# Optimization experiments

Hardware: AMD Instinct MI355X
Metric: run time of the kernel (lower is better)

## Reference

```python
import jax, jax.numpy as jnp
import numpy as np

N, E, G = 40000, 640000, 32
H, HEADS, L, O = 128, 4, 4, 100
C = H // HEADS


def setup_inputs() -> dict:
    key = jax.random.key(0)
    ks = iter(jax.random.split(key, 40))
    def w(shape, fan):
        return jax.random.normal(next(ks), shape, jnp.float32) / np.float32(np.sqrt(fan))
    inp = {}
    inp["x"] = jax.random.normal(next(ks), (N, 4), jnp.float32)
    inp["edge_attr"] = jax.random.normal(next(ks), (E, 5), jnp.float32)
    inp["node_w"] = w((4, H), 4); inp["node_b"] = jnp.zeros((H,), jnp.float32)
    inp["edge_w"] = w((5, H), 5); inp["edge_b"] = jnp.zeros((H,), jnp.float32)
    inp["Wq"] = w((L, H, H), H); inp["bq"] = jnp.zeros((L, H), jnp.float32)
    inp["Wk"] = w((L, H, H), H); inp["bk"] = jnp.zeros((L, H), jnp.float32)
    inp["Wv"] = w((L, H, H), H); inp["bv"] = jnp.zeros((L, H), jnp.float32)
    inp["We"] = w((L, H, H), H)  # lin_edge has bias=False in PyG TransformerConv
    inp["Wskip"] = w((L, H, H), H); inp["bskip"] = jnp.zeros((L, H), jnp.float32)
    inp["ln_g"] = jnp.ones((L, H), jnp.float32); inp["ln_b"] = jnp.zeros((L, H), jnp.float32)
    inp["dos_w1"] = w((H, H // 2), H); inp["dos_b1"] = jnp.zeros((H // 2,), jnp.float32)
    inp["dos_w2"] = w((H // 2, O), H // 2); inp["dos_b2"] = jnp.zeros((O,), jnp.float32)
    inp["tr_w1"] = w((H, H // 2), H); inp["tr_b1"] = jnp.zeros((H // 2,), jnp.float32)
    inp["tr_w2"] = w((H // 2, O), H // 2); inp["tr_b2"] = jnp.zeros((O,), jnp.float32)
    inp["edge_index"] = jax.random.randint(next(ks), (2, E), 0, N, jnp.int32)
    inp["batch"] = jnp.sort(jax.random.randint(next(ks), (N,), 0, G, jnp.int32))
    return inp


def _seg_softmax(a, seg, n):
    # numerically stable scatter-softmax over edges grouped by destination node
    m = jax.ops.segment_max(a, seg, num_segments=n)
    e = jnp.exp(a - m[seg])
    s = jax.ops.segment_sum(e, seg, num_segments=n)
    return e / (s[seg] + 1e-16)


def _layer_norm(x, g, b, eps=1e-5):
    mu = x.mean(-1, keepdims=True)
    var = ((x - mu) ** 2).mean(-1, keepdims=True)
    return (x - mu) * jax.lax.rsqrt(var + eps) * g + b


def _forward(x, edge_attr, node_w, node_b, edge_w, edge_b, Wq, bq, Wk, bk, Wv, bv,
             We, Wskip, bskip, ln_g, ln_b,
             dos_w1, dos_b1, dos_w2, dos_b2, tr_w1, tr_b1, tr_w2, tr_b2,
             edge_index, batch):
    src, dst = edge_index[0], edge_index[1]  # PyG default flow: source->target
    n = x.shape[0]
    h = x @ node_w + node_b        # [N, H] node_proj
    e_h = edge_attr @ edge_w + edge_b  # [E, H] edge_proj (shared across layers)
    scale = np.float32(1.0 / np.sqrt(C))
    for i in range(L):  # TransformerConv -> LayerNorm -> ReLU (dropout is eval-mode no-op)
        q = (h @ Wq[i] + bq[i]).reshape(n, HEADS, C)
        k = (h @ Wk[i] + bk[i]).reshape(n, HEADS, C)
        v = (h @ Wv[i] + bv[i]).reshape(n, HEADS, C)
        e = (e_h @ We[i]).reshape(-1, HEADS, C)
        kj = k[src] + e            # [E, heads, C]
        vj = v[src] + e
        alpha = jnp.sum(q[dst] * kj, axis=-1) * scale  # [E, heads]
        alpha = _seg_softmax(alpha, dst, n)
        msg = vj * alpha[..., None]
        out = jax.ops.segment_sum(msg, dst, num_segments=n).reshape(n, H)
        out = out + h @ Wskip[i] + bskip[i]  # root_weight skip
        h = jax.nn.relu(_layer_norm(out, ln_g[i], ln_b[i]))
    # global mean pool per graph
    sums = jax.ops.segment_sum(h, batch, num_segments=G)
    cnt = jax.ops.segment_sum(jnp.ones((n, 1), h.dtype), batch, num_segments=G)
    hg = sums / jnp.maximum(cnt, 1.0)
    dos = jax.nn.relu(hg @ dos_w1 + dos_b1) @ dos_w2 + dos_b2
    tr = jax.nn.relu(hg @ tr_w1 + tr_b1) @ tr_w2 + tr_b2
    return dos, tr


def reference(x, edge_attr, node_w, node_b, edge_w, edge_b, Wq, bq, Wk, bk, Wv, bv,
              We, Wskip, bskip, ln_g, ln_b,
              dos_w1, dos_b1, dos_w2, dos_b2, tr_w1, tr_b1, tr_w2, tr_b2,
              edge_index, batch):
    return _forward(x, edge_attr, node_w, node_b, edge_w, edge_b, Wq, bq, Wk, bk, Wv, bv,
                    We, Wskip, bskip, ln_g, ln_b,
                    dos_w1, dos_b1, dos_w2, dos_b2, tr_w1, tr_b1, tr_w2, tr_b2,
                    edge_index, batch)
```

## Files before the change

kernel.cpp:

```cpp
#include <hip/hip_runtime.h>
#include <hip/hip_fp16.h>
#include <math.h>

#define N_NODES 40000
#define N_EDGES 640000
#define N_GRAPHS 32
#define HDIM 128
#define NHEADS 4
#define CDIM 32
#define NLAYERS 4
#define ODIM 100
#define SCAN_B 256
#define SCAN_NBLK ((N_NODES + SCAN_B - 1) / SCAN_B)
#define M_PAD 40064
#define POOL_CHUNK 32
#define POOL_NBLK ((N_NODES + POOL_CHUNK - 1) / POOL_CHUNK)
#define SCALE 0.17677669529663687f

typedef __bf16 bf16_t;
typedef bf16_t bf16x8 __attribute__((ext_vector_type(8)));
typedef float f32x4 __attribute__((ext_vector_type(4)));
typedef _Float16 h2v __attribute__((ext_vector_type(2)));

#if defined(__has_builtin)
#if __has_builtin(__builtin_amdgcn_fdot2)
#define HAVE_FDOT2 1
#endif
#endif

struct __align__(8) H2P { __half2 k; __half2 v; };

__global__ void nodeproj_kernel(const float* __restrict__ x,
                                const float* __restrict__ w,
                                const float* __restrict__ b,
                                bf16_t* __restrict__ hb) {
    int idx = blockIdx.x * blockDim.x + threadIdx.x;
    if (idx >= N_NODES * HDIM) return;
    int n = idx >> 7, c = idx & 127;
    float s = b[c];
    s += x[n * 4 + 0] * w[0 * HDIM + c];
    s += x[n * 4 + 1] * w[1 * HDIM + c];
    s += x[n * 4 + 2] * w[2 * HDIM + c];
    s += x[n * 4 + 3] * w[3 * HDIM + c];
    hb[idx] = (bf16_t)s;
}

__global__ void fold_edge_kernel(const float* __restrict__ edge_w,
                                 const float* __restrict__ edge_b,
                                 const float* __restrict__ We,
                                 float* __restrict__ Me_all,
                                 float* __restrict__ ce_all) {
    int blk = blockIdx.x;
    int i = blk / 6, j = blk % 6;
    int c = threadIdx.x;
    const float* W = We + (size_t)i * HDIM * HDIM;
    float s = 0.0f;
    if (j < 5) {
        for (int k = 0; k < HDIM; ++k) s += edge_w[j * HDIM + k] * W[k * HDIM + c];
        Me_all[i * 5 * HDIM + j * HDIM + c] = s;
    } else {
        for (int k = 0; k < HDIM; ++k) s += edge_b[k] * W[k * HDIM + c];
        ce_all[i * HDIM + c] = s;
    }
}

__global__ void count_deg_kernel(const int* __restrict__ ei, int* __restrict__ deg) {
    int e = blockIdx.x * blockDim.x + threadIdx.x;
    if (e >= N_EDGES) return;
    atomicAdd(&deg[ei[N_EDGES + e]], 1);
}

__global__ void scan1_kernel(const int* __restrict__ deg,
                             int* __restrict__ rowptr, int* __restrict__ bsum) {
    __shared__ int sd[SCAN_B];
    int tid = threadIdx.x;
    int i = blockIdx.x * SCAN_B + tid;
    int v = (i < N_NODES) ? deg[i] : 0;
    sd[tid] = v;
    __syncthreads();
#pragma unroll
    for (int off = 1; off < SCAN_B; off <<= 1) {
        int tmp = (tid >= off) ? sd[tid - off] : 0;
        __syncthreads();
        sd[tid] += tmp;
        __syncthreads();
    }
    if (i < N_NODES) rowptr[i] = sd[tid] - v;
    if (tid == SCAN_B - 1) bsum[blockIdx.x] = sd[tid];
}

__global__ void scan2_kernel(const int* __restrict__ bsum, int* __restrict__ bscan) {
    __shared__ int sd[SCAN_B];
    int tid = threadIdx.x;
    int v = (tid < SCAN_NBLK) ? bsum[tid] : 0;
    sd[tid] = v;
    __syncthreads();
#pragma unroll
    for (int off = 1; off < SCAN_B; off <<= 1) {
        int tmp = (tid >= off) ? sd[tid - off] : 0;
        __syncthreads();
        sd[tid] += tmp;
        __syncthreads();
    }
    if (tid < SCAN_NBLK) bscan[tid] = sd[tid] - v;
}

__global__ void scan3_kernel(int* __restrict__ rowptr, const int* __restrict__ bscan) {
    int i = blockIdx.x * SCAN_B + threadIdx.x;
    if (i < N_NODES) rowptr[i] += bscan[blockIdx.x];
    if (i == 0) rowptr[N_NODES] = N_EDGES;
}

__global__ void fill_csr_kernel(const int* __restrict__ ei,
                                const float* __restrict__ ea,
                                const int* __restrict__ rowptr,
                                int* __restrict__ cursor,
                                int* __restrict__ srcarr,
                                float* __restrict__ ea8) {
    int e = blockIdx.x * blockDim.x + threadIdx.x;
    if (e >= N_EDGES) return;
    int src = ei[e], dst = ei[N_EDGES + e];
    int pos = atomicAdd(&cursor[dst], 1);
    int p = rowptr[dst] + pos;
    srcarr[p] = src;
    float4 lo = make_float4(ea[(size_t)e * 5 + 0], ea[(size_t)e * 5 + 1],
                            ea[(size_t)e * 5 + 2], ea[(size_t)e * 5 + 3]);
    float4 hi = make_float4(ea[(size_t)e * 5 + 4], 0.f, 0.f, 0.f);
    *(float4*)(ea8 + (size_t)p * 8)     = lo;
    *(float4*)(ea8 + (size_t)p * 8 + 4) = hi;
}

__global__ void convert_w_kernel(const float* __restrict__ Wq, const float* __restrict__ Wk,
                                 const float* __restrict__ Wv, const float* __restrict__ Ws,
                                 bf16_t* __restrict__ Wtb) {
    int b = blockIdx.x;
    int n = b & 127;
    int matli = b >> 7;
    int mat = matli & 3, li = matli >> 2;
    int kk = threadIdx.x;
    const float* W = (mat == 0 ? Wq : mat == 1 ? Wk : mat == 2 ? Wv : Ws) + (size_t)li * HDIM * HDIM;
    float val = W[kk * HDIM + n];
    if (mat == 1) val *= SCALE;
    Wtb[((size_t)(li * 4 + mat) * HDIM + n) * HDIM + kk] = (bf16_t)val;
}

__global__ __launch_bounds__(512) void gemm_mfma(
    const bf16_t* __restrict__ hb, const bf16_t* __restrict__ Wt,
    const float* __restrict__ bq, const float* __restrict__ bk,
    const float* __restrict__ bv, const float* __restrict__ bs,
    __half2* __restrict__ q2o, H2P* __restrict__ kv2o,
    float* __restrict__ so) {
    __shared__ bf16_t Ash[128 * 128];
    __shared__ bf16_t Bsh[128 * 128];
    int tid = threadIdx.x;
    int mt = blockIdx.y;
    int row0 = blockIdx.x * 128;

    {
        const bf16_t* W0 = Wt + (size_t)(mt == 0 ? 0 : (mt == 1 ? 1 : 3)) * HDIM * HDIM;
#pragma unroll
        for (int p = 0; p < 4; ++p) {
            int i = tid + p * 512;
            int rr = i >> 4, g = i & 15;
            int sw = (g ^ (rr & 15)) << 3;
            *(bf16x8*)(Ash + rr * 128 + sw) = *(const bf16x8*)(hb + (size_t)(row0 + rr) * HDIM + g * 8);
            *(bf16x8*)(Bsh + rr * 128 + sw) = *(const bf16x8*)(W0 + (size_t)rr * HDIM + g * 8);
        }
    }
    __syncthreads();

    int lane = tid & 63, wave = tid >> 6;
    int wr = (wave >> 2) * 64, wc = (wave & 3) * 32;
    int lm = lane & 15, quad = lane >> 4;

    f32x4 acc[4][2];
#pragma unroll
    for (int i = 0; i < 4; ++i)
#pragma unroll
        for (int j = 0; j < 2; ++j) acc[i][j] = (f32x4){0.f, 0.f, 0.f, 0.f};

#pragma unroll
    for (int ks = 0; ks < 4; ++ks) {
        int gg = ks * 4 + quad;
        int sw = (gg ^ lm) << 3;
        bf16x8 af[4], bf[2];
#pragma unroll
        for (int t = 0; t < 4; ++t)
            af[t] = *(const bf16x8*)(Ash + (wr + t * 16 + lm) * 128 + sw);
#pragma unroll
        for (int j = 0; j < 2; ++j)
            bf[j] = *(const bf16x8*)(Bsh + (wc + j * 16 + lm) * 128 + sw);
#pragma unroll
        for (int i = 0; i < 4; ++i)
#pragma unroll
            for (int j = 0; j < 2; ++j)
                acc[i][j] = __builtin_amdgcn_mfma_f32_16x16x32_bf16(af[i], bf[j], acc[i][j], 0, 0, 0);
    }

    int c0 = wc + lm;
    int pi = ((wave & 3) << 4) | lm;

    if (mt == 0) {
        float b0 = bq[c0], b1 = bq[c0 + 16];
#pragma unroll
        for (int i = 0; i < 4; ++i) {
            int rbase = row0 + wr + i * 16 + quad * 4;
#pragma unroll
            for (int r = 0; r < 4; ++r) {
                int row = rbase + r;
                if (row < N_NODES)
                    q2o[(size_t)row * 64 + pi] =
                        __floats2half2_rn(acc[i][0][r] + b0, acc[i][1][r] + b1);
            }
        }
    } else if (mt == 1) {
        f32x4 acc2[4][2];
#pragma unroll
        for (int i = 0; i < 4; ++i)
#pragma unroll
            for (int j = 0; j < 2; ++j) acc2[i][j] = (f32x4){0.f, 0.f, 0.f, 0.f};
        __syncthreads();
        {
            const bf16_t* W1 = Wt + (size_t)2 * HDIM * HDIM;
#pragma unroll
            for (int p = 0; p < 4; ++p) {
                int i = tid + p * 512;
                int rr = i >> 4, g = i & 15;
                int sw = (g ^ (rr & 15)) << 3;
                *(bf16x8*)(Bsh + rr * 128 + sw) = *(const bf16x8*)(W1 + (size_t)rr * HDIM + g * 8);
            }
        }
        __syncthreads();
#pragma unroll
        for (int ks = 0; ks < 4; ++ks) {
            int gg = ks * 4 + quad;
            int sw = (gg ^ lm) << 3;
            bf16x8 af[4], bf[2];
#pragma unroll
            for (int t = 0; t < 4; ++t)
                af[t] = *(const bf16x8*)(Ash + (wr + t * 16 + lm) * 128 + sw);
#pragma unroll
            for (int j = 0; j < 2; ++j)
                bf[j] = *(const bf16x8*)(Bsh + (wc + j * 16 + lm) * 128 + sw);
#pragma unroll
            for (int i = 0; i < 4; ++i)
#pragma unroll
                for (int j = 0; j < 2; ++j)
                    acc2[i][j] = __builtin_amdgcn_mfma_f32_16x16x32_bf16(af[i], bf[j], acc2[i][j], 0, 0, 0);
        }
        float kb0 = bk[c0] * SCALE, kb1 = bk[c0 + 16] * SCALE;
        float vb0 = bv[c0], vb1 = bv[c0 + 16];
#pragma unroll
        for (int i = 0; i < 4; ++i) {
            int rbase = row0 + wr + i * 16 + quad * 4;
#pragma unroll
            for (int r = 0; r < 4; ++r) {
                int row = rbase + r;
                if (row < N_NODES) {
                    H2P h;
                    h.k = __floats2half2_rn(acc[i][0][r] + kb0, acc[i][1][r] + kb1);
                    h.v = __floats2half2_rn(acc2[i][0][r] + vb0, acc2[i][1][r] + vb1);
                    kv2o[(size_t)row * 64 + pi] = h;
                }
            }
        }
    } else {
        float b0 = bs[c0], b1 = bs[c0 + 16];
#pragma unroll
        for (int i = 0; i < 4; ++i) {
            int rbase = row0 + wr + i * 16 + quad * 4;
#pragma unroll
            for (int r = 0; r < 4; ++r) {
                int row = rbase + r;
                if (row < N_NODES) {
                    so[(size_t)row * HDIM + c0]      = acc[i][0][r] + b0;
                    so[(size_t)row * HDIM + c0 + 16] = acc[i][1][r] + b1;
                }
            }
        }
    }
}

__global__ __launch_bounds__(128) void agg_kernel(
    const int* __restrict__ srcarr, const int* __restrict__ rowptr,
    const float* __restrict__ ea8,
    const __half2* __restrict__ q2,
    const H2P* __restrict__ kv2,
    const float* __restrict__ Me, const float* __restrict__ ce,
    const float* __restrict__ skip,
    const float* __restrict__ lg, const float* __restrict__ lb,
    bf16_t* __restrict__ hbout) {
    int t = threadIdx.x & 63;
    int n = blockIdx.x * 2 + (threadIdx.x >> 6);
    int cc = t & 15;
    int clo = ((t >> 4) << 5) | cc;
    int chi = clo + 16;

    __half2 qh = q2[(size_t)n * 64 + t];
    float2 qf = __half22float2(qh);
    float cwlo = ce[clo], cwhi = ce[chi];
    float mlo[5], mhi[5];
#pragma unroll
    for (int j = 0; j < 5; ++j) { mlo[j] = Me[j * HDIM + clo]; mhi[j] = Me[j * HDIM + chi]; }

    float myq = 0.0f;
#pragma unroll
    for (int j = 0; j < 6; ++j) {
        float a = (j < 5) ? mlo[j] : cwlo;
        float b = (j < 5) ? mhi[j] : cwhi;
        float p = (qf.x * a + qf.y * b) * SCALE;
        p += __shfl_xor(p, 8, 16);
        p += __shfl_xor(p, 4, 16);
        p += __shfl_xor(p, 2, 16);
        p += __shfl_xor(p, 1, 16);
        if (cc == j) myq = p;
    }

    int beg = rowptr[n], end = rowptr[n + 1];
    float l[4], o0[4], o1[4], ab[4];
#pragma unroll
    for (int s = 0; s < 4; ++s) { l[s] = 0.f; o0[s] = 0.f; o1[s] = 0.f; ab[s] = 0.f; }

    if (beg < end) {
        int e1 = end - 1;
        int srcB[4];
        float avA[4], avB[4];
        H2P kvA[4];
        {
            int srcA[4];
#pragma unroll
            for (int s = 0; s < 4; ++s) {
                int ca = beg + s;       ca = (ca < e1) ? ca : e1;
                int cb = beg + 4 + s;   cb = (cb < e1) ? cb : e1;
                srcA[s] = srcarr[ca];
                srcB[s] = srcarr[cb];
                avA[s] = (cc < 5) ? ea8[(size_t)ca * 8 + cc] : 1.0f;
                avB[s] = (cc < 5) ? ea8[(size_t)cb * 8 + cc] : 1.0f;
            }
#pragma unroll
            for (int s = 0; s < 4; ++s) kvA[s] = kv2[(size_t)srcA[s] * 64 + t];
        }

        for (int base = beg; base < end; base += 4) {
            H2P kvB[4];
#pragma unroll
            for (int s = 0; s < 4; ++s) kvB[s] = kv2[(size_t)srcB[s] * 64 + t];
            int srcC[4]; float avC[4];
#pragma unroll
            for (int s = 0; s < 4; ++s) {
                int cidx = base + 8 + s; cidx = (cidx < e1) ? cidx : e1;
                srcC[s] = srcarr[cidx];
                avC[s] = (cc < 5) ? ea8[(size_t)cidx * 8 + cc] : 1.0f;
            }
            float p4[4], vx[4], vy[4];
#pragma unroll
            for (int s = 0; s < 4; ++s) {
                float2 vf = __half22float2(kvA[s].v);
                vx[s] = vf.x; vy[s] = vf.y;
                float pa = myq * avA[s];
#if defined(HAVE_FDOT2)
                p4[s] = __builtin_amdgcn_fdot2(__builtin_bit_cast(h2v, qh),
                                               __builtin_bit_cast(h2v, kvA[s].k), pa, false);
#else
                float2 kf = __half22float2(kvA[s].k);
                p4[s] = fmaf(qf.x, kf.x, fmaf(qf.y, kf.y, pa));
#endif
            }
#pragma unroll
            for (int st = 8; st >= 1; st >>= 1) {
#pragma unroll
                for (int s = 0; s < 4; ++s) p4[s] += __shfl_xor(p4[s], st, 16);
            }
#pragma unroll
            for (int s = 0; s < 4; ++s) {
                float pe = (base + s < end) ? __expf(p4[s]) : 0.0f;
                o0[s] = fmaf(pe, vx[s], o0[s]);
                o1[s] = fmaf(pe, vy[s], o1[s]);
                l[s] += pe;
                ab[s] = fmaf(pe, avA[s], ab[s]);
            }
#pragma unroll
            for (int s = 0; s < 4; ++s) {
                kvA[s] = kvB[s];
                avA[s] = avB[s];
                srcB[s] = srcC[s];
                avB[s] = avC[s];
            }
        }
    }
    float lt  = (l[0] + l[1]) + (l[2] + l[3]);
    float o0t = (o0[0] + o0[1]) + (o0[2] + o0[3]);
    float o1t = (o1[0] + o1[1]) + (o1[2] + o1[3]);
    float abt = (ab[0] + ab[1]) + (ab[2] + ab[3]);

    float nlo = fmaf(lt, cwlo, o0t);
    float nhi = fmaf(lt, cwhi, o1t);
#pragma unroll
    for (int j = 0; j < 5; ++j) {
        float abj = __shfl(abt, (t & 48) + j, 64);
        nlo = fmaf(mlo[j], abj, nlo);
        nhi = fmaf(mhi[j], abj, nhi);
    }
    float inv = 1.0f / (lt + 1e-16f);
    float vlo = skip[(size_t)n * HDIM + clo] + nlo * inv;
    float vhi = skip[(size_t)n * HDIM + chi] + nhi * inv;

    float s = vlo + vhi;
#pragma unroll
    for (int mask = 32; mask >= 1; mask >>= 1) s += __shfl_xor(s, mask, 64);
    float mu = s * (1.0f / HDIM);
    float dlo = vlo - mu, dhi = vhi - mu;
    float s2 = dlo * dlo + dhi * dhi;
#pragma unroll
    for (int mask = 32; mask >= 1; mask >>= 1) s2 += __shfl_xor(s2, mask, 64);
    float rstd = rsqrtf(s2 * (1.0f / HDIM) + 1e-5f);
    float ylo = fmaxf(dlo * rstd * lg[clo] + lb[clo], 0.0f);
    float yhi = fmaxf(dhi * rstd * lg[chi] + lb[chi], 0.0f);
    hbout[(size_t)n * HDIM + clo] = (bf16_t)ylo;
    hbout[(size_t)n * HDIM + chi] = (bf16_t)yhi;
}

__global__ __launch_bounds__(128) void pool_kernel(const bf16_t* __restrict__ h,
                                                   const int* __restrict__ batch,
                                                   float* __restrict__ pool,
                                                   float* __restrict__ cnt) {
    int t = threadIdx.x;
    int n0 = blockIdx.x * POOL_CHUNK;
    int n1 = n0 + POOL_CHUNK;
    if (n1 > N_NODES) n1 = N_NODES;
    int gcur = batch[n0];
    int cstart = n0;
    float acc = 0.0f;
    for (int n = n0; n < n1; ++n) {
        int g = batch[n];
        if (g != gcur) {
            atomicAdd(&pool[gcur * HDIM + t], acc);
            if (t == 0) atomicAdd(&cnt[gcur], (float)(n - cstart));
            acc = 0.0f;
            gcur = g;
            cstart = n;
        }
        acc += (float)h[(size_t)n * HDIM + t];
    }
    atomicAdd(&pool[gcur * HDIM + t], acc);
    if (t == 0) atomicAdd(&cnt[gcur], (float)(n1 - cstart));
}

__global__ void heads_kernel(const float* __restrict__ pool,
                             const float* __restrict__ cnt,
                             const float* __restrict__ dw1, const float* __restrict__ db1,
                             const float* __restrict__ dw2, const float* __restrict__ db2,
                             const float* __restrict__ tw1, const float* __restrict__ tb1,
                             const float* __restrict__ tw2, const float* __restrict__ tb2,
                             float* __restrict__ outp) {
    int g = blockIdx.x, t = threadIdx.x;
    __shared__ float hg[HDIM];
    __shared__ float hid[64];
    float c = fmaxf(cnt[g], 1.0f);
    hg[t] = pool[g * HDIM + t] / c;
    __syncthreads();
    if (t < 64) {
        float s = db1[t];
        for (int i = 0; i < HDIM; ++i) s += hg[i] * dw1[i * 64 + t];
        hid[t] = fmaxf(s, 0.0f);
    }
    __syncthreads();
    if (t < ODIM) {
        float s = db2[t];
        for (int j = 0; j < 64; ++j) s += hid[j] * dw2[j * ODIM + t];
        outp[g * ODIM + t] = s;
    }
    __syncthreads();
    if (t < 64) {
        float s = tb1[t];
        for (int i = 0; i < HDIM; ++i) s += hg[i] * tw1[i * 64 + t];
        hid[t] = fmaxf(s, 0.0f);
    }
    __syncthreads();
    if (t < ODIM) {
        float s = tb2[t];
        for (int j = 0; j < 64; ++j) s += hid[j] * tw2[j * ODIM + t];
        outp[N_GRAPHS * ODIM + g * ODIM + t] = s;
    }
}

extern "C" void kernel_launch(void* const* d_in, const int* in_sizes, int n_in,
                              void* d_out, int out_size, void* d_ws, size_t ws_size,
                              hipStream_t stream) {
    const float* x        = (const float*)d_in[0];
    const float* ea       = (const float*)d_in[1];
    const float* node_w   = (const float*)d_in[2];
    const float* node_b   = (const float*)d_in[3];
    const float* edge_w   = (const float*)d_in[4];
    const float* edge_b   = (const float*)d_in[5];
    const float* Wq       = (const float*)d_in[6];
    const float* bq       = (const float*)d_in[7];
    const float* Wk       = (const float*)d_in[8];
    const float* bk       = (const float*)d_in[9];
    const float* Wv       = (const float*)d_in[10];
    const float* bv       = (const float*)d_in[11];
    const float* We       = (const float*)d_in[12];
    const float* Wskip    = (const float*)d_in[13];
    const float* bskip    = (const float*)d_in[14];
    const float* ln_g     = (const float*)d_in[15];
    const float* ln_b     = (const float*)d_in[16];
    const float* dw1      = (const float*)d_in[17];
    const float* db1      = (const float*)d_in[18];
    const float* dw2      = (const float*)d_in[19];
    const float* db2      = (const float*)d_in[20];
    const float* tw1      = (const float*)d_in[21];
    const float* tb1      = (const float*)d_in[22];
    const float* tw2      = (const float*)d_in[23];
    const float* tb2      = (const float*)d_in[24];
    const int*   ei       = (const int*)d_in[25];
    const int*   batch    = (const int*)d_in[26];
    float* out = (float*)d_out;
    (void)in_sizes; (void)n_in; (void)out_size; (void)ws_size;

    char* wsb = (char*)d_ws;
    size_t off = 0;
    auto carve = [&](size_t bytes) -> void* {
        void* p = wsb + off;
        off += (bytes + 255) & ~(size_t)255;
        return p;
    };
    bf16_t*  hbuf   = (bf16_t*) carve((size_t)M_PAD * HDIM * 2);
    __half2* q2b    = (__half2*)carve((size_t)N_NODES * 64 * 4);
    H2P*     kv2b   = (H2P*)    carve((size_t)N_NODES * 64 * 8);
    float*   ob     = (float*)  carve((size_t)N_NODES * HDIM * 4);
    bf16_t*  Wtb    = (bf16_t*) carve((size_t)NLAYERS * 4 * HDIM * HDIM * 2);
    int*     srcarr = (int*)    carve((size_t)N_EDGES * 4);
    float*   ea8    = (float*)  carve((size_t)N_EDGES * 8 * 4);
    int*     deg    = (int*)    carve((size_t)N_NODES * 4);
    int*     cursor = (int*)    carve((size_t)N_NODES * 4);
    int*     rowptr = (int*)    carve((size_t)(N_NODES + 1) * 4);
    int*     bsum   = (int*)    carve((size_t)SCAN_NBLK * 4);
    int*     bscan  = (int*)    carve((size_t)SCAN_NBLK * 4);
    float*   Me_all = (float*)  carve((size_t)NLAYERS * 5 * HDIM * 4);
    float*   ce_all = (float*)  carve((size_t)NLAYERS * HDIM * 4);
    float*   pool   = (float*)  carve((size_t)N_GRAPHS * HDIM * 4);
    float*   cnt    = (float*)  carve((size_t)N_GRAPHS * 4);

    const int nthreads = 256;
    const int e_blocks  = (N_EDGES + nthreads - 1) / nthreads;
    const int nc_blocks = (N_NODES * HDIM) / nthreads;

    hipMemsetAsync(deg, 0, (size_t)N_NODES * 4 * 2, stream);
    count_deg_kernel<<<e_blocks, nthreads, 0, stream>>>(ei, deg);
    scan1_kernel<<<SCAN_NBLK, SCAN_B, 0, stream>>>(deg, rowptr, bsum);
    scan2_kernel<<<1, SCAN_B, 0, stream>>>(bsum, bscan);
    scan3_kernel<<<SCAN_NBLK, SCAN_B, 0, stream>>>(rowptr, bscan);
    fill_csr_kernel<<<e_blocks, nthreads, 0, stream>>>(ei, ea, rowptr, cursor, srcarr, ea8);

    hipMemsetAsync(hbuf + (size_t)N_NODES * HDIM, 0,
                   (size_t)(M_PAD - N_NODES) * HDIM * 2, stream);
    nodeproj_kernel<<<nc_blocks, nthreads, 0, stream>>>(x, node_w, node_b, hbuf);
    fold_edge_kernel<<<NLAYERS * 6, HDIM, 0, stream>>>(edge_w, edge_b, We, Me_all, ce_all);
    convert_w_kernel<<<NLAYERS * 4 * HDIM, HDIM, 0, stream>>>(Wq, Wk, Wv, Wskip, Wtb);

    for (int i = 0; i < NLAYERS; ++i) {
        const float* Me = Me_all + i * 5 * HDIM;
        const float* ce = ce_all + i * HDIM;
        gemm_mfma<<<dim3(M_PAD / 128, 3), 512, 0, stream>>>(
            hbuf, Wtb + (size_t)i * 4 * HDIM * HDIM,
            bq + i * HDIM, bk + i * HDIM, bv + i * HDIM, bskip + i * HDIM,
            q2b, kv2b, ob);
        agg_kernel<<<N_NODES / 2, 128, 0, stream>>>(srcarr, rowptr, ea8, q2b, kv2b,
                                                    Me, ce, ob,
                                                    ln_g + i * HDIM, ln_b + i * HDIM, hbuf);
    }

    hipMemsetAsync(pool, 0, (size_t)(N_GRAPHS * HDIM + N_GRAPHS) * 4, stream);
    pool_kernel<<<POOL_NBLK, HDIM, 0, stream>>>(hbuf, batch, pool, cnt);
    heads_kernel<<<N_GRAPHS, HDIM, 0, stream>>>(pool, cnt, dw1, db1, dw2, db2,
                                                tw1, tb1, tw2, tb2, out);
}
```

Baseline: 546.3 us.

## Compute all four projections per 64-row tile, reusing staged activations

```diff
diff --git a/kernel.cpp b/kernel.cpp
--- a/kernel.cpp
+++ b/kernel.cpp
@@ -144,67 +144,98 @@
     Wtb[((size_t)(li * 4 + mat) * HDIM + n) * HDIM + kk] = (bf16_t)val;
 }
 
-__global__ __launch_bounds__(512) void gemm_mfma(
+__global__ __launch_bounds__(256) void gemm_mfma(
     const bf16_t* __restrict__ hb, const bf16_t* __restrict__ Wt,
     const float* __restrict__ bq, const float* __restrict__ bk,
     const float* __restrict__ bv, const float* __restrict__ bs,
     __half2* __restrict__ q2o, H2P* __restrict__ kv2o,
     float* __restrict__ so) {
-    __shared__ bf16_t Ash[128 * 128];
+    __shared__ bf16_t Ash[64 * 128];
     __shared__ bf16_t Bsh[128 * 128];
     int tid = threadIdx.x;
-    int mt = blockIdx.y;
-    int row0 = blockIdx.x * 128;
+    int row0 = blockIdx.x * 64;
 
     {
-        const bf16_t* W0 = Wt + (size_t)(mt == 0 ? 0 : (mt == 1 ? 1 : 3)) * HDIM * HDIM;
 #pragma unroll
         for (int p = 0; p < 4; ++p) {
-            int i = tid + p * 512;
+            int i = tid + p * 256;
             int rr = i >> 4, g = i & 15;
             int sw = (g ^ (rr & 15)) << 3;
-            *(bf16x8*)(Ash + rr * 128 + sw) = *(const bf16x8*)(hb + (size_t)(row0 + rr) * HDIM + g * 8);
-            *(bf16x8*)(Bsh + rr * 128 + sw) = *(const bf16x8*)(W0 + (size_t)rr * HDIM + g * 8);
-        }
-    }
-    __syncthreads();
+            *(bf16x8*)(Ash + rr * 128 + sw) =
+                *(const bf16x8*)(hb + (size_t)(row0 + rr) * HDIM + g * 8);
+        }
+    }
 
     int lane = tid & 63, wave = tid >> 6;
-    int wr = (wave >> 2) * 64, wc = (wave & 3) * 32;
     int lm = lane & 15, quad = lane >> 4;
-
-    f32x4 acc[4][2];
-#pragma unroll
-    for (int i = 0; i < 4; ++i)
-#pragma unroll
-        for (int j = 0; j < 2; ++j) acc[i][j] = (f32x4){0.f, 0.f, 0.f, 0.f};
-
-#pragma unroll
-    for (int ks = 0; ks < 4; ++ks) {
-        int gg = ks * 4 + quad;
-        int sw = (gg ^ lm) << 3;
-        bf16x8 af[4], bf[2];
-#pragma unroll
-        for (int t = 0; t < 4; ++t)
-            af[t] = *(const bf16x8*)(Ash + (wr + t * 16 + lm) * 128 + sw);
-#pragma unroll
-        for (int j = 0; j < 2; ++j)
-            bf[j] = *(const bf16x8*)(Bsh + (wc + j * 16 + lm) * 128 + sw);
+    int wc = wave * 32;
+    int c0 = wc + lm;
+    int pi = (wave << 4) | lm;
+
+    auto stageB = [&](int mat) {
+        const bf16_t* W = Wt + (size_t)mat * HDIM * HDIM;
+#pragma unroll
+        for (int p = 0; p < 8; ++p) {
+            int i = tid + p * 256;
+            int rr = i >> 4, g = i & 15;
+            int sw = (g ^ (rr & 15)) << 3;
+            *(bf16x8*)(Bsh + rr * 128 + sw) = *(const bf16x8*)(W + (size_t)rr * HDIM + g * 8);
+        }
+    };
+    auto runMat = [&](f32x4 acc[4][2]) {
 #pragma unroll
         for (int i = 0; i < 4; ++i)
 #pragma unroll
+            for (int j = 0; j < 2; ++j) acc[i][j] = (f32x4){0.f, 0.f, 0.f, 0.f};
+#pragma unroll
+        for (int ks = 0; ks < 4; ++ks) {
+            int gg = ks * 4 + quad;
+            int sw = (gg ^ lm) << 3;
+            bf16x8 af[4], bf[2];
+#pragma unroll
+            for (int t = 0; t < 4; ++t)
+                af[t] = *(const bf16x8*)(Ash + (t * 16 + lm) * 128 + sw);
+#pragma unroll
             for (int j = 0; j < 2; ++j)
-                acc[i][j] = __builtin_amdgcn_mfma_f32_16x16x32_bf16(af[i], bf[j], acc[i][j], 0, 0, 0);
-    }
-
-    int c0 = wc + lm;
-    int pi = ((wave & 3) << 4) | lm;
-
-    if (mt == 0) {
+                bf[j] = *(const bf16x8*)(Bsh + (wc + j * 16 + lm) * 128 + sw);
+#pragma unroll
+            for (int i = 0; i < 4; ++i)
+#pragma unroll
+                for (int j = 0; j < 2; ++j)
+                    acc[i][j] = __builtin_amdgcn_mfma_f32_16x16x32_bf16(af[i], bf[j], acc[i][j], 0, 0, 0);
+        }
+    };
+
+    f32x4 acc[4][2], kacc[4][2];
+
+    stageB(3);
+    __syncthreads();
+    runMat(acc);
+    {
+        float b0 = bs[c0], b1 = bs[c0 + 16];
+#pragma unroll
+        for (int i = 0; i < 4; ++i) {
+            int rbase = row0 + i * 16 + quad * 4;
+#pragma unroll
+            for (int r = 0; r < 4; ++r) {
+                int row = rbase + r;
+                if (row < N_NODES) {
+                    so[(size_t)row * HDIM + c0]      = acc[i][0][r] + b0;
+                    so[(size_t)row * HDIM + c0 + 16] = acc[i][1][r] + b1;
+                }
+            }
+        }
+    }
+    __syncthreads();
+
+    stageB(0);
+    __syncthreads();
+    runMat(acc);
+    {
         float b0 = bq[c0], b1 = bq[c0 + 16];
 #pragma unroll
         for (int i = 0; i < 4; ++i) {
-            int rbase = row0 + wr + i * 16 + quad * 4;
+            int rbase = row0 + i * 16 + quad * 4;
 #pragma unroll
             for (int r = 0; r < 4; ++r) {
                 int row = rbase + r;
@@ -213,68 +244,31 @@
                         __floats2half2_rn(acc[i][0][r] + b0, acc[i][1][r] + b1);
             }
         }
-    } else if (mt == 1) {
-        f32x4 acc2[4][2];
-#pragma unroll
-        for (int i = 0; i < 4; ++i)
-#pragma unroll
-            for (int j = 0; j < 2; ++j) acc2[i][j] = (f32x4){0.f, 0.f, 0.f, 0.f};
-        __syncthreads();
-        {
-            const bf16_t* W1 = Wt + (size_t)2 * HDIM * HDIM;
-#pragma unroll
-            for (int p = 0; p < 4; ++p) {
-                int i = tid + p * 512;
-                int rr = i >> 4, g = i & 15;
-                int sw = (g ^ (rr & 15)) << 3;
-                *(bf16x8*)(Bsh + rr * 128 + sw) = *(const bf16x8*)(W1 + (size_t)rr * HDIM + g * 8);
-            }
-        }
-        __syncthreads();
-#pragma unroll
-        for (int ks = 0; ks < 4; ++ks) {
-            int gg = ks * 4 + quad;
-            int sw = (gg ^ lm) << 3;
-            bf16x8 af[4], bf[2];
-#pragma unroll
-            for (int t = 0; t < 4; ++t)
-                af[t] = *(const bf16x8*)(Ash + (wr + t * 16 + lm) * 128 + sw);
-#pragma unroll
-            for (int j = 0; j < 2; ++j)
-                bf[j] = *(const bf16x8*)(Bsh + (wc + j * 16 + lm) * 128 + sw);
-#pragma unroll
-            for (int i = 0; i < 4; ++i)
-#pragma unroll
-                for (int j = 0; j < 2; ++j)
-                    acc2[i][j] = __builtin_amdgcn_mfma_f32_16x16x32_bf16(af[i], bf[j], acc2[i][j], 0, 0, 0);
-        }
+    }
+    __syncthreads();
+
+    stageB(1);
+    __syncthreads();
+    runMat(kacc);
+    __syncthreads();
+
+    stageB(2);
+    __syncthreads();
+    runMat(acc);
+    {
         float kb0 = bk[c0] * SCALE, kb1 = bk[c0 + 16] * SCALE;
         float vb0 = bv[c0], vb1 = bv[c0 + 16];
 #pragma unroll
         for (int i = 0; i < 4; ++i) {
-            int rbase = row0 + wr + i * 16 + quad * 4;
+            int rbase = row0 + i * 16 + quad * 4;
 #pragma unroll
             for (int r = 0; r < 4; ++r) {
                 int row = rbase + r;
                 if (row < N_NODES) {
                     H2P h;
-                    h.k = __floats2half2_rn(acc[i][0][r] + kb0, acc[i][1][r] + kb1);
-                    h.v = __floats2half2_rn(acc2[i][0][r] + vb0, acc2[i][1][r] + vb1);
+                    h.k = __floats2half2_rn(kacc[i][0][r] + kb0, kacc[i][1][r] + kb1);
+                    h.v = __floats2half2_rn(acc[i][0][r] + vb0, acc[i][1][r] + vb1);
                     kv2o[(size_t)row * 64 + pi] = h;
-                }
-            }
-        }
-    } else {
-        float b0 = bs[c0], b1 = bs[c0 + 16];
-#pragma unroll
-        for (int i = 0; i < 4; ++i) {
-            int rbase = row0 + wr + i * 16 + quad * 4;
-#pragma unroll
-            for (int r = 0; r < 4; ++r) {
-                int row = rbase + r;
-                if (row < N_NODES) {
-                    so[(size_t)row * HDIM + c0]      = acc[i][0][r] + b0;
-                    so[(size_t)row * HDIM + c0 + 16] = acc[i][1][r] + b1;
                 }
             }
         }
@@ -561,7 +555,7 @@
     for (int i = 0; i < NLAYERS; ++i) {
         const float* Me = Me_all + i * 5 * HDIM;
         const float* ce = ce_all + i * HDIM;
-        gemm_mfma<<<dim3(M_PAD / 128, 3), 512, 0, stream>>>(
+        gemm_mfma<<<M_PAD / 64, 256, 0, stream>>>(
             hbuf, Wtb + (size_t)i * 4 * HDIM * HDIM,
             bq + i * HDIM, bk + i * HDIM, bv + i * HDIM, bskip + i * HDIM,
             q2b, kv2b, ob);
```

Result: slower. 596.9 us (+9.3%).
